# Kernel tuning notes

Hardware: AMD Instinct MI355X
Metric: run time of the kernel (lower is better)

Reference implementation:

```python
import jax, jax.numpy as jnp
import numpy as np

B, F, C, T, K, P = 16, 32, 32, 2048, 129, 64  # P = conv padding; K-1-P = 64 -> same-length output


def setup_inputs() -> dict:
    key = jax.random.key(0)
    k0, k1, k2, k3, k4, k5 = jax.random.split(key, 6)
    coeffs = jax.random.normal(k0, (B, 2, F, 7, 5, T), dtype=jnp.float32)
    rows = jax.random.randint(k1, (C,), 0, 7, dtype=jnp.int32)
    cols = jax.random.randint(k2, (C,), 0, 5, dtype=jnp.int32)
    ri_scale = jax.random.uniform(k3, (F,), jnp.float32, 0.5, 1.5)
    ri_shift = jax.random.normal(k4, (F,), dtype=jnp.float32) * 0.1
    freq_gain = jnp.ones((F,), dtype=jnp.float32)
    # torch ConvTranspose1d weight: (in_channels=C*2F, out_channels/groups=1, K)
    synth_weight = jax.random.normal(k5, (C * 2 * F, 1, K), dtype=jnp.float32) / np.sqrt(2.0 * F * K)
    return {"coeffs": coeffs, "rows": rows, "cols": cols, "ri_scale": ri_scale,
            "ri_shift": ri_shift, "freq_gain": freq_gain, "synth_weight": synth_weight}


def reference(coeffs, rows, cols, ri_scale, ri_shift, freq_gain, synth_weight):
    Bc, _, Fq, _, _, Tt = coeffs.shape
    Cc = rows.shape[0]
    # fancy-index gather over the (7,5) electrode grid -> (B, 2, F, C, T)
    feat = coeffs[:, :, :, rows, cols, :]
    # normalize (ri stats broadcast over freq dim) then per-frequency gain
    fdim = (None, None, slice(None), None, None)
    feat = feat / (ri_scale[fdim] + 1e-12) - ri_shift[fdim]
    feat = feat * freq_gain[fdim]
    # permute (B,2,F,C,T) -> (B,C,2,F,T) and flatten to (B, C*2F, T)
    z = jnp.transpose(feat, (0, 3, 1, 2, 4)).reshape(Bc, Cc * 2 * Fq, Tt)
    # depthwise-grouped ConvTranspose1d (stride=1, padding=P) == grouped
    # cross-correlation with time-flipped kernel and padding K-1-P.
    Kk = synth_weight.shape[-1]
    w = synth_weight.reshape(Cc, 2 * Fq, Kk)[:, :, ::-1]  # (Cout=C, Cin/groups=2F, K)
    pad = Kk - 1 - P
    x_hat = jax.lax.conv_general_dilated(
        z, w, window_strides=(1,), padding=[(pad, pad)],
        feature_group_count=Cc, dimension_numbers=("NCH", "OIH", "NCH"))
    return x_hat  # (B, C, T)
```

## Files before the change

kernel.cpp:

```cpp
#include <hip/hip_runtime.h>

typedef __attribute__((ext_vector_type(8))) short short8;
typedef __attribute__((ext_vector_type(4))) float f32x4;

#define C_ 32
#define T_ 2048
#define K_ 129

__device__ __forceinline__ unsigned int bfround(float f) {
    unsigned int u = __float_as_uint(f);
    return u + 0x7fffu + ((u >> 16) & 1u);
}

#define BARRIER_LDS() do {                                   \
    __builtin_amdgcn_sched_barrier(0);                       \
    asm volatile("s_waitcnt lgkmcnt(0)" ::: "memory");       \
    __builtin_amdgcn_s_barrier();                            \
    __builtin_amdgcn_sched_barrier(0);                       \
} while (0)

__global__ __launch_bounds__(256) void wtoep_pack(
    const float* __restrict__ sw, unsigned short* __restrict__ wt)
{
    const int c = blockIdx.x, dd = blockIdx.y;
    const int t = threadIdx.x, l = t & 63, fw = t >> 6;
    const int m = l & 15, qb = (l >> 4) & 1, i2 = (l >> 5) & 1;
    const int d = dd - 4;
    for (int fr = fw; fr < 32; fr += 4) {
        const int iq = fr >> 2, igl = fr & 3;
        const int i = iq * 8 + igl * 2 + i2;
        unsigned short v[8];
        #pragma unroll
        for (int e = 0; e < 8; ++e) {
            const int tl = 8 * qb + e;
            const int j = 16 * d + 64 + m - tl;
            const float wv = (j >= 0 && j <= 128) ? sw[(c * 64 + i) * K_ + j] : 0.f;
            v[e] = (unsigned short)(bfround(wv) >> 16);
        }
        *(short8*)(wt + (((c * 9 + dd) * 32 + fr) * 64 + l) * 8) = *(short8*)v;
    }
}

__global__ __launch_bounds__(256, 2) void wavelet_synth_v6(
    const float* __restrict__ coeffs, const int* __restrict__ rows,
    const int* __restrict__ cols, const float* __restrict__ ri_scale,
    const float* __restrict__ ri_shift, const float* __restrict__ freq_gain,
    const unsigned short* __restrict__ wt, float* __restrict__ out)
{
    __shared__ __align__(16) unsigned char smem[65536];
    unsigned short* zs = (unsigned short*)smem;

    const int t  = threadIdx.x;
    const int g0 = blockIdx.x * 8;
    const int c  = blockIdx.y;
    const int rc = rows[c];
    const int cc = cols[c];

    const int lane = t & 63;
    const int w    = t >> 6;
    const int i2   = (lane >> 5) & 1;
    const int qb   = (lane >> 4) & 1;

    const int s_r  = t & 1;
    const int s_b  = (t >> 1) & 15;
    const int s_il = (t >> 5) & 7;

    f32x4 acc[16];
    #pragma unroll
    for (int a = 0; a < 16; ++a) acc[a] = (f32x4){0.f, 0.f, 0.f, 0.f};

    float4 pf[16];
    {
        const int i  = s_il;
        const int f  = i & 31;
        const int ri = i >> 5;
        const long row = ((long)(s_b * 2 + ri) * 32 + f) * 35 + rc * 5 + cc;
        const float* src = coeffs + row * T_ + g0 * 16 + s_r * 8;
        #pragma unroll
        for (int vi = 0; vi < 8; ++vi) {
            pf[vi * 2 + 0] = *(const float4*)(src + vi * 16);
            pf[vi * 2 + 1] = *(const float4*)(src + vi * 16 + 4);
        }
    }

    for (int iq = 0; iq < 8; ++iq) {
        const int i = iq * 8 + s_il;
        const int f = i & 31;
        const float inv = __builtin_amdgcn_rcpf(ri_scale[f] + 1e-12f);
        const float Aa  = inv * freq_gain[f];
        const float Bb  = -ri_shift[f] * freq_gain[f];

        BARRIER_LDS();

        #pragma unroll
        for (int vi = 0; vi < 8; ++vi) {
            const float4 x = pf[vi * 2 + 0];
            const float4 y = pf[vi * 2 + 1];
            float vv[8];
            vv[0] = x.x * Aa + Bb; vv[1] = x.y * Aa + Bb;
            vv[2] = x.z * Aa + Bb; vv[3] = x.w * Aa + Bb;
            vv[4] = y.x * Aa + Bb; vv[5] = y.y * Aa + Bb;
            vv[6] = y.z * Aa + Bb; vv[7] = y.w * Aa + Bb;
            unsigned short pk[8];
            #pragma unroll
            for (int e = 0; e < 8; ++e) pk[e] = (unsigned short)(bfround(vv[e]) >> 16);
            *(short8*)(zs + ((vi * 8 + s_il) * 16 + s_b) * 24 + s_r * 8) = *(short8*)pk;
        }

        if (iq < 7) {
            const int i1  = (iq + 1) * 8 + s_il;
            const int f1  = i1 & 31;
            const int ri1 = i1 >> 5;
            const long row1 = ((long)(s_b * 2 + ri1) * 32 + f1) * 35 + rc * 5 + cc;
            const float* src1 = coeffs + row1 * T_ + g0 * 16 + s_r * 8;
            #pragma unroll
            for (int vi = 0; vi < 8; ++vi) {
                pf[vi * 2 + 0] = *(const float4*)(src1 + vi * 16);
                pf[vi * 2 + 1] = *(const float4*)(src1 + vi * 16 + 4);
            }
        }

        BARRIER_LDS();

        const unsigned short* wbase = wt + ((c * 9) * 32 + iq * 4 + w) * 512 + lane * 8;
        const unsigned short* zb =
            zs + ((w * 2 + i2) * 16 + (lane & 15)) * 24 + qb * 8;
        short8 bfr[8];
        #pragma unroll
        for (int vi = 0; vi < 8; ++vi)
            bfr[vi] = *(const short8*)(zb + vi * (8 * 16 * 24));
        #pragma unroll
        for (int d = 0; d < 9; ++d) {
            const short8 afrag = *(const short8*)(wbase + d * 32 * 512);
            #pragma unroll
            for (int vi = 0; vi < 8; ++vi) {
                acc[vi + d] = __builtin_amdgcn_mfma_f32_16x16x32_bf16(
                    afrag, bfr[vi], acc[vi + d], 0, 0, 0);
            }
        }
    }

    BARRIER_LDS();
    float* red = (float*)smem;
    #pragma unroll
    for (int a = 0; a < 16; ++a)
        *(f32x4*)(red + ((w * 16 + a) * 64 + lane) * 4) = acc[a];
    BARRIER_LDS();

    {
        const int rb  = t >> 4;
        const int tau = t & 15;
        const int s   = tau >> 2;
        const int rr  = tau & 3;
        float* obase = out + ((long)rb * C_ + c) * T_ + tau;
        #pragma unroll
        for (int a = 0; a < 16; ++a) {
            const int o = g0 - 4 + a;
            if (o < 0 || o >= 128) continue;
            float sum = 0.f;
            #pragma unroll
            for (int ww = 0; ww < 4; ++ww)
                sum += red[((ww * 16 + a) * 64 + s * 16 + rb) * 4 + rr];
            unsafeAtomicAdd(obase + o * 16, sum);
        }
    }
}

extern "C" void kernel_launch(void* const* d_in, const int* in_sizes, int n_in,
                              void* d_out, int out_size, void* d_ws, size_t ws_size,
                              hipStream_t stream) {
    const float* coeffs    = (const float*)d_in[0];
    const int*   rows      = (const int*)d_in[1];
    const int*   cols      = (const int*)d_in[2];
    const float* ri_scale  = (const float*)d_in[3];
    const float* ri_shift  = (const float*)d_in[4];
    const float* freq_gain = (const float*)d_in[5];
    const float* sw        = (const float*)d_in[6];
    float* out = (float*)d_out;
    unsigned short* wt = (unsigned short*)d_ws;

    hipMemsetAsync(d_out, 0, (size_t)out_size, stream);
    hipLaunchKernelGGL(wtoep_pack, dim3(32, 9), dim3(256), 0, stream, sw, wt);
    hipLaunchKernelGGL(wavelet_synth_v6, dim3(16, 32), dim3(256), 0, stream,
                       coeffs, rows, cols, ri_scale, ri_shift, freq_gain, wt, out);
}
```

Measured before the change: 398.2 us.

## Double-buffer LDS staging with XOR swizzle and prefetch two stages ahead

The main kernel now keeps two LDS buffers for the packed bf16 activations. The next tile is normalized and written while the current tile's MFMAs run, and global loads are issued two iterations ahead, which drops one barrier per iteration. The padded LDS stride of 24 is replaced by an XOR-swizzled dense layout to avoid bank conflicts. The weight pack kernel is split across twice as many blocks. In exchange the kernel uses more LDS, and keeping the prefetched registers live during the MFMA phase may raise register pressure under the two-blocks-per-CU launch bound.

```diff
diff --git a/kernel.cpp b/kernel.cpp
--- a/kernel.cpp
+++ b/kernel.cpp
@@ -22,11 +22,11 @@
 __global__ __launch_bounds__(256) void wtoep_pack(
     const float* __restrict__ sw, unsigned short* __restrict__ wt)
 {
-    const int c = blockIdx.x, dd = blockIdx.y;
+    const int c = blockIdx.x, dd = blockIdx.y, bz = blockIdx.z;
     const int t = threadIdx.x, l = t & 63, fw = t >> 6;
     const int m = l & 15, qb = (l >> 4) & 1, i2 = (l >> 5) & 1;
     const int d = dd - 4;
-    for (int fr = fw; fr < 32; fr += 4) {
+    for (int fr = fw + 16 * bz; fr < 16 * bz + 16; fr += 4) {
         const int iq = fr >> 2, igl = fr & 3;
         const int i = iq * 8 + igl * 2 + i2;
         unsigned short v[8];
@@ -41,14 +41,19 @@
     }
 }
 
-__global__ __launch_bounds__(256, 2) void wavelet_synth_v6(
+__device__ __forceinline__ int zidx(int R, int half) {
+    return (R * 16 + half * 8) ^ (((R >> 2) & 7) << 3);
+}
+
+__global__ __launch_bounds__(256, 2) void wavelet_synth_v7(
     const float* __restrict__ coeffs, const int* __restrict__ rows,
     const int* __restrict__ cols, const float* __restrict__ ri_scale,
     const float* __restrict__ ri_shift, const float* __restrict__ freq_gain,
     const unsigned short* __restrict__ wt, float* __restrict__ out)
 {
     __shared__ __align__(16) unsigned char smem[65536];
-    unsigned short* zs = (unsigned short*)smem;
+    unsigned short* const zs0 = (unsigned short*)smem;
+    unsigned short* const zs1 = zs0 + 16384;
 
     const int t  = threadIdx.x;
     const int g0 = blockIdx.x * 8;
@@ -65,70 +70,65 @@
     const int s_b  = (t >> 1) & 15;
     const int s_il = (t >> 5) & 7;
 
+    const int wr_off = zidx(s_il * 16 + s_b, s_r);
+    const int rd_off = zidx((w * 2 + i2) * 16 + (lane & 15), qb);
+
     f32x4 acc[16];
     #pragma unroll
     for (int a = 0; a < 16; ++a) acc[a] = (f32x4){0.f, 0.f, 0.f, 0.f};
 
     float4 pf[16];
-    {
-        const int i  = s_il;
-        const int f  = i & 31;
-        const int ri = i >> 5;
-        const long row = ((long)(s_b * 2 + ri) * 32 + f) * 35 + rc * 5 + cc;
-        const float* src = coeffs + row * T_ + g0 * 16 + s_r * 8;
-        #pragma unroll
-        for (int vi = 0; vi < 8; ++vi) {
-            pf[vi * 2 + 0] = *(const float4*)(src + vi * 16);
-            pf[vi * 2 + 1] = *(const float4*)(src + vi * 16 + 4);
-        }
-    }
+
+#define LOADPF(J) do {                                                        \
+    const int i_ = (J) * 8 + s_il;                                            \
+    const int f_ = i_ & 31, ri_ = i_ >> 5;                                    \
+    const long row_ = ((long)(s_b * 2 + ri_) * 32 + f_) * 35 + rc * 5 + cc;   \
+    const float* src_ = coeffs + row_ * T_ + g0 * 16 + s_r * 8;               \
+    _Pragma("unroll")                                                         \
+    for (int vi = 0; vi < 8; ++vi) {                                          \
+        pf[vi * 2 + 0] = *(const float4*)(src_ + vi * 16);                    \
+        pf[vi * 2 + 1] = *(const float4*)(src_ + vi * 16 + 4);                \
+    }                                                                         \
+} while (0)
+
+#define PACK(J, DST) do {                                                     \
+    const int i_ = (J) * 8 + s_il;                                            \
+    const int f_ = i_ & 31;                                                   \
+    const float inv_ = __builtin_amdgcn_rcpf(ri_scale[f_] + 1e-12f);          \
+    const float Aa_  = inv_ * freq_gain[f_];                                  \
+    const float Bb_  = -ri_shift[f_] * freq_gain[f_];                         \
+    _Pragma("unroll")                                                         \
+    for (int vi = 0; vi < 8; ++vi) {                                          \
+        const float4 x_ = pf[vi * 2 + 0];                                     \
+        const float4 y_ = pf[vi * 2 + 1];                                     \
+        float vv_[8];                                                         \
+        vv_[0] = x_.x * Aa_ + Bb_; vv_[1] = x_.y * Aa_ + Bb_;                 \
+        vv_[2] = x_.z * Aa_ + Bb_; vv_[3] = x_.w * Aa_ + Bb_;                 \
+        vv_[4] = y_.x * Aa_ + Bb_; vv_[5] = y_.y * Aa_ + Bb_;                 \
+        vv_[6] = y_.z * Aa_ + Bb_; vv_[7] = y_.w * Aa_ + Bb_;                 \
+        unsigned short pk_[8];                                                \
+        _Pragma("unroll")                                                     \
+        for (int e = 0; e < 8; ++e) pk_[e] = (unsigned short)(bfround(vv_[e]) >> 16); \
+        *(short8*)((DST) + wr_off + vi * 2048) = *(short8*)pk_;               \
+    }                                                                         \
+} while (0)
+
+    LOADPF(0);
+    PACK(0, zs0);
+    LOADPF(1);
+
+    unsigned short* zcur = zs0;
+    unsigned short* znxt = zs1;
 
     for (int iq = 0; iq < 8; ++iq) {
-        const int i = iq * 8 + s_il;
-        const int f = i & 31;
-        const float inv = __builtin_amdgcn_rcpf(ri_scale[f] + 1e-12f);
-        const float Aa  = inv * freq_gain[f];
-        const float Bb  = -ri_shift[f] * freq_gain[f];
-
-        BARRIER_LDS();
-
-        #pragma unroll
-        for (int vi = 0; vi < 8; ++vi) {
-            const float4 x = pf[vi * 2 + 0];
-            const float4 y = pf[vi * 2 + 1];
-            float vv[8];
-            vv[0] = x.x * Aa + Bb; vv[1] = x.y * Aa + Bb;
-            vv[2] = x.z * Aa + Bb; vv[3] = x.w * Aa + Bb;
-            vv[4] = y.x * Aa + Bb; vv[5] = y.y * Aa + Bb;
-            vv[6] = y.z * Aa + Bb; vv[7] = y.w * Aa + Bb;
-            unsigned short pk[8];
-            #pragma unroll
-            for (int e = 0; e < 8; ++e) pk[e] = (unsigned short)(bfround(vv[e]) >> 16);
-            *(short8*)(zs + ((vi * 8 + s_il) * 16 + s_b) * 24 + s_r * 8) = *(short8*)pk;
-        }
-
-        if (iq < 7) {
-            const int i1  = (iq + 1) * 8 + s_il;
-            const int f1  = i1 & 31;
-            const int ri1 = i1 >> 5;
-            const long row1 = ((long)(s_b * 2 + ri1) * 32 + f1) * 35 + rc * 5 + cc;
-            const float* src1 = coeffs + row1 * T_ + g0 * 16 + s_r * 8;
-            #pragma unroll
-            for (int vi = 0; vi < 8; ++vi) {
-                pf[vi * 2 + 0] = *(const float4*)(src1 + vi * 16);
-                pf[vi * 2 + 1] = *(const float4*)(src1 + vi * 16 + 4);
-            }
-        }
-
         BARRIER_LDS();
 
         const unsigned short* wbase = wt + ((c * 9) * 32 + iq * 4 + w) * 512 + lane * 8;
-        const unsigned short* zb =
-            zs + ((w * 2 + i2) * 16 + (lane & 15)) * 24 + qb * 8;
+        const unsigned short* zb = zcur + rd_off;
         short8 bfr[8];
         #pragma unroll
         for (int vi = 0; vi < 8; ++vi)
-            bfr[vi] = *(const short8*)(zb + vi * (8 * 16 * 24));
+            bfr[vi] = *(const short8*)(zb + vi * 2048);
         #pragma unroll
         for (int d = 0; d < 9; ++d) {
             const short8 afrag = *(const short8*)(wbase + d * 32 * 512);
@@ -138,6 +138,11 @@
                     afrag, bfr[vi], acc[vi + d], 0, 0, 0);
             }
         }
+
+        if (iq < 7) PACK(iq + 1, znxt);
+        if (iq < 6) LOADPF(iq + 2);
+
+        unsigned short* tmp = zcur; zcur = znxt; znxt = tmp;
     }
 
     BARRIER_LDS();
@@ -164,6 +169,8 @@
             unsafeAtomicAdd(obase + o * 16, sum);
         }
     }
+#undef LOADPF
+#undef PACK
 }
 
 extern "C" void kernel_launch(void* const* d_in, const int* in_sizes, int n_in,
@@ -180,7 +187,7 @@
     unsigned short* wt = (unsigned short*)d_ws;
 
     hipMemsetAsync(d_out, 0, (size_t)out_size, stream);
-    hipLaunchKernelGGL(wtoep_pack, dim3(32, 9), dim3(256), 0, stream, sw, wt);
-    hipLaunchKernelGGL(wavelet_synth_v6, dim3(16, 32), dim3(256), 0, stream,
+    hipLaunchKernelGGL(wtoep_pack, dim3(32, 9, 2), dim3(256), 0, stream, sw, wt);
+    hipLaunchKernelGGL(wavelet_synth_v7, dim3(16, 32), dim3(256), 0, stream,
                        coeffs, rows, cols, ri_scale, ri_shift, freq_gain, wt, out);
 }
```

Result: no change. 392.6 us (-1.4%).
